# Kernel tuning notes

Hardware: AMD Instinct MI355X
Metric: run time of the kernel (lower is better)

The kernel has to match this reference:

```python
import jax, jax.numpy as jnp
import numpy as np

BATCH, IN, HID, OUT = 8192, 1024, 2048, 1024


def setup_inputs() -> dict:
    key = jax.random.key(0)
    ks = jax.random.split(key, 13)
    s = 0.02
    return {
        "x": jax.random.normal(ks[0], (BATCH, IN), jnp.float32),
        "hidden": jax.random.normal(ks[1], (BATCH, HID), jnp.float32),
        # torch nn.Linear stores weight as (out_features, in_features)
        "Wxr_w": jax.random.normal(ks[2], (HID, IN), jnp.float32) * s,
        "Wxr_b": jax.random.normal(ks[3], (HID,), jnp.float32) * s,
        "Whr_w": jax.random.normal(ks[4], (HID, HID), jnp.float32) * s,
        "Wxz_w": jax.random.normal(ks[5], (HID, IN), jnp.float32) * s,
        "Wxz_b": jax.random.normal(ks[6], (HID,), jnp.float32) * s,
        "Whz_w": jax.random.normal(ks[7], (HID, HID), jnp.float32) * s,
        "Wxh_w": jax.random.normal(ks[8], (HID, IN), jnp.float32) * s,
        "Wxh_b": jax.random.normal(ks[9], (HID,), jnp.float32) * s,
        "Whh_w": jax.random.normal(ks[10], (HID, HID), jnp.float32) * s,
        "Who_w": jax.random.normal(ks[11], (OUT, HID), jnp.float32) * s,
        "Who_b": jax.random.normal(ks[12], (OUT,), jnp.float32) * s,
    }


def _lin(x, w, b=None):
    y = x @ w.T
    return y if b is None else y + b


def reference(x, hidden, Wxr_w, Wxr_b, Whr_w, Wxz_w, Wxz_b, Whz_w,
              Wxh_w, Wxh_b, Whh_w, Who_w, Who_b):
    # GRU cell, one timestep
    r = jax.nn.sigmoid(_lin(x, Wxr_w, Wxr_b) + _lin(hidden, Whr_w))      # reset gate (B,H)
    z = jax.nn.sigmoid(_lin(x, Wxz_w, Wxz_b) + _lin(hidden, Whz_w))      # update gate (B,H)
    h_cand = jnp.tanh(_lin(x, Wxh_w, Wxh_b) + _lin(r * hidden, Whh_w))    # candidate (B,H)
    new_hidden = z * hidden + (1.0 - z) * h_cand                          # blend (B,H)
    output = _lin(new_hidden, Who_w, Who_b)                               # (B,OUT)
    return (output, new_hidden)
```

## Files before the change

### kernel.cpp

```cpp
#include <hip/hip_runtime.h>
#include <hip/hip_bf16.h>
#include <stdint.h>

typedef __bf16 bf16_t;
typedef __bf16 bf16x8 __attribute__((ext_vector_type(8)));
typedef float f32x4 __attribute__((ext_vector_type(4)));

#define B_SZ   8192
#define D_IN   1024
#define D_HID  2048
#define D_OUT  1024

#define BM 128
#define BN 128
#define BK 64

struct CastJobs {
  const float* src[9];
  bf16_t* dst[9];
  int n8[9];
};

__global__ __launch_bounds__(256) void cast_kernel(CastJobs j) {
  const int which = blockIdx.y;
  const int t = blockIdx.x * 256 + threadIdx.x;
  if (t >= j.n8[which]) return;
  const float4* s = (const float4*)j.src[which];
  float4 a = s[2 * t], b = s[2 * t + 1];
  bf16x8 o;
  o[0] = (bf16_t)a.x; o[1] = (bf16_t)a.y; o[2] = (bf16_t)a.z; o[3] = (bf16_t)a.w;
  o[4] = (bf16_t)b.x; o[5] = (bf16_t)b.y; o[6] = (bf16_t)b.z; o[7] = (bf16_t)b.w;
  *(bf16x8*)(j.dst[which] + (size_t)t * 8) = o;
}

__device__ __forceinline__ void stage_tile(const bf16_t* __restrict__ src, int ld,
                                           int row_base, int col_base,
                                           char* tile, int wid, int lane) {
#pragma unroll
  for (int i = 0; i < 4; ++i) {
    int p = i * 4096 + wid * 1024 + lane * 16;
    int row = p >> 7;
    int chunk = ((p >> 4) & 7) ^ (row & 7);
    const bf16_t* g = src + (size_t)(row_base + row) * ld + col_base + chunk * 8;
    __builtin_amdgcn_global_load_lds(
        (const __attribute__((address_space(1))) void*)g,
        (__attribute__((address_space(3))) void*)(tile + i * 4096 + wid * 1024),
        16, 0, 0);
  }
}

__device__ __forceinline__ bf16x8 read_frag(const char* tile, int row, int k) {
  int slot = (k >> 3) ^ (row & 7);
  return *(const bf16x8*)(tile + row * 128 + slot * 16);
}

__device__ __forceinline__ float sigm(float x) { return 1.0f / (1.0f + __expf(-x)); }

template <int MODE>
__global__ __launch_bounds__(256, 2) void gru_gemm(
    const bf16_t* __restrict__ xb, const bf16_t* __restrict__ hb,
    const bf16_t* __restrict__ wxr, const bf16_t* __restrict__ whr,
    const bf16_t* __restrict__ wxz, const bf16_t* __restrict__ whz,
    const bf16_t* __restrict__ wxh, const bf16_t* __restrict__ whh,
    const bf16_t* __restrict__ who,
    const float* __restrict__ bxr, const float* __restrict__ bxz,
    const float* __restrict__ bxh, const float* __restrict__ bwo,
    const float* __restrict__ hidden_f32,
    bf16_t* __restrict__ rh, bf16_t* __restrict__ zb, bf16_t* __restrict__ hx,
    bf16_t* __restrict__ nhb, float* __restrict__ out_y, float* __restrict__ out_nh) {
  __shared__ char lds[32768];
  char* sA = lds;
  char* sB = lds + 16384;

  const int tid = threadIdx.x;
  const int wid = tid >> 6;
  const int lane = tid & 63;
  const int wr = wid >> 1, wc = wid & 1;
  const int l15 = lane & 15, lq = lane >> 4;

  const int bm = blockIdx.x * BM;
  int region = 0, bn;
  if (MODE == 0) { region = blockIdx.y >> 4; bn = (blockIdx.y & 15) * BN; }
  else bn = blockIdx.y * BN;

  int KT;
  const bf16_t *BX = nullptr, *BH = nullptr;
  if (MODE == 0) {
    if (region == 0)      { BX = wxr; BH = whr; KT = D_IN + D_HID; }
    else if (region == 1) { BX = wxz; BH = whz; KT = D_IN + D_HID; }
    else                  { BX = wxh;           KT = D_IN; }
  } else {
    KT = D_HID;
  }

  f32x4 acc[4][4];
#pragma unroll
  for (int i = 0; i < 4; ++i)
#pragma unroll
    for (int j = 0; j < 4; ++j) acc[i][j] = (f32x4){0.f, 0.f, 0.f, 0.f};

  for (int kt = 0; kt < KT; kt += BK) {
    const bf16_t *As, *Bs;
    int lda, ldb, ac, bc;
    if (MODE == 0) {
      if (kt < D_IN) { As = xb; lda = D_IN;  ac = kt;        Bs = BX; ldb = D_IN;  bc = kt; }
      else           { As = hb; lda = D_HID; ac = kt - D_IN; Bs = BH; ldb = D_HID; bc = kt - D_IN; }
    } else if (MODE == 1) { As = rh;  lda = D_HID; ac = kt; Bs = whh; ldb = D_HID; bc = kt; }
    else                  { As = nhb; lda = D_HID; ac = kt; Bs = who; ldb = D_HID; bc = kt; }

    stage_tile(As, lda, bm, ac, sA, wid, lane);
    stage_tile(Bs, ldb, bn, bc, sB, wid, lane);
    asm volatile("s_waitcnt vmcnt(0)" ::: "memory");
    __syncthreads();

#pragma unroll
    for (int kk = 0; kk < BK; kk += 32) {
      bf16x8 af[4], bfr[4];
      const int k = kk + lq * 8;
#pragma unroll
      for (int i = 0; i < 4; ++i) af[i]  = read_frag(sA, wr * 64 + i * 16 + l15, k);
#pragma unroll
      for (int i = 0; i < 4; ++i) bfr[i] = read_frag(sB, wc * 64 + i * 16 + l15, k);
#pragma unroll
      for (int mi = 0; mi < 4; ++mi)
#pragma unroll
        for (int ni = 0; ni < 4; ++ni)
          acc[mi][ni] = __builtin_amdgcn_mfma_f32_16x16x32_bf16(af[mi], bfr[ni], acc[mi][ni], 0, 0, 0);
    }
    __syncthreads();
  }

#pragma unroll
  for (int ni = 0; ni < 4; ++ni) {
    const int col = bn + wc * 64 + ni * 16 + l15;
#pragma unroll
    for (int mi = 0; mi < 4; ++mi) {
      const int row0 = bm + wr * 64 + mi * 16 + lq * 4;
#pragma unroll
      for (int j = 0; j < 4; ++j) {
        const int row = row0 + j;
        const float v = acc[mi][ni][j];
        if (MODE == 0) {
          const size_t off = (size_t)row * D_HID + col;
          if (region == 0) {
            float rr = sigm(v + bxr[col]);
            rh[off] = (bf16_t)(rr * hidden_f32[off]);
          } else if (region == 1) {
            zb[off] = (bf16_t)sigm(v + bxz[col]);
          } else {
            hx[off] = (bf16_t)(v + bxh[col]);
          }
        } else if (MODE == 1) {
          const size_t off = (size_t)row * D_HID + col;
          float hc = tanhf((float)hx[off] + v);
          float z = (float)zb[off];
          float h = hidden_f32[off];
          float nh = z * h + (1.0f - z) * hc;
          out_nh[off] = nh;
          nhb[off] = (bf16_t)nh;
        } else {
          out_y[(size_t)row * D_OUT + col] = v + bwo[col];
        }
      }
    }
  }
}

extern "C" void kernel_launch(void* const* d_in, const int* in_sizes, int n_in,
                              void* d_out, int out_size, void* d_ws, size_t ws_size,
                              hipStream_t stream) {
  const float* x   = (const float*)d_in[0];
  const float* hid = (const float*)d_in[1];
  const float* Wxr = (const float*)d_in[2];
  const float* bxr = (const float*)d_in[3];
  const float* Whr = (const float*)d_in[4];
  const float* Wxz = (const float*)d_in[5];
  const float* bxz = (const float*)d_in[6];
  const float* Whz = (const float*)d_in[7];
  const float* Wxh = (const float*)d_in[8];
  const float* bxh = (const float*)d_in[9];
  const float* Whh = (const float*)d_in[10];
  const float* Who = (const float*)d_in[11];
  const float* bwo = (const float*)d_in[12];

  float* out_y  = (float*)d_out;
  float* out_nh = out_y + (size_t)B_SZ * D_OUT;

  char* w = (char*)d_ws;
  auto alloc = [&](size_t bytes) { char* p = w; w += (bytes + 255) & ~(size_t)255; return p; };

  bf16_t* xb  = (bf16_t*)alloc((size_t)B_SZ * D_IN * 2);
  bf16_t* hb  = (bf16_t*)alloc((size_t)B_SZ * D_HID * 2);
  bf16_t* wxr = (bf16_t*)alloc((size_t)D_HID * D_IN * 2);
  bf16_t* whr = (bf16_t*)alloc((size_t)D_HID * D_HID * 2);
  bf16_t* wxz = (bf16_t*)alloc((size_t)D_HID * D_IN * 2);
  bf16_t* whz = (bf16_t*)alloc((size_t)D_HID * D_HID * 2);
  bf16_t* wxh = (bf16_t*)alloc((size_t)D_HID * D_IN * 2);
  bf16_t* whh = (bf16_t*)alloc((size_t)D_HID * D_HID * 2);
  bf16_t* who = (bf16_t*)alloc((size_t)D_OUT * D_HID * 2);
  bf16_t* rh  = (bf16_t*)alloc((size_t)B_SZ * D_HID * 2);
  bf16_t* zb  = (bf16_t*)alloc((size_t)B_SZ * D_HID * 2);
  bf16_t* hx  = (bf16_t*)alloc((size_t)B_SZ * D_HID * 2);
  bf16_t* nhb = (bf16_t*)alloc((size_t)B_SZ * D_HID * 2);

  CastJobs cj;
  const float* srcs[9] = {x, hid, Wxr, Whr, Wxz, Whz, Wxh, Whh, Who};
  bf16_t* dsts[9]      = {xb, hb, wxr, whr, wxz, whz, wxh, whh, who};
  const int ns[9] = {B_SZ * D_IN, B_SZ * D_HID,
                     D_HID * D_IN, D_HID * D_HID,
                     D_HID * D_IN, D_HID * D_HID,
                     D_HID * D_IN, D_HID * D_HID,
                     D_OUT * D_HID};
  for (int i = 0; i < 9; ++i) { cj.src[i] = srcs[i]; cj.dst[i] = dsts[i]; cj.n8[i] = ns[i] / 8; }

  cast_kernel<<<dim3(8192, 9), dim3(256), 0, stream>>>(cj);

  dim3 blk(256);
  gru_gemm<0><<<dim3(64, 48), blk, 0, stream>>>(xb, hb, wxr, whr, wxz, whz, wxh, whh, who,
                                                bxr, bxz, bxh, bwo, hid,
                                                rh, zb, hx, nhb, out_y, out_nh);
  gru_gemm<1><<<dim3(64, 16), blk, 0, stream>>>(xb, hb, wxr, whr, wxz, whz, wxh, whh, who,
                                                bxr, bxz, bxh, bwo, hid,
                                                rh, zb, hx, nhb, out_y, out_nh);
  gru_gemm<2><<<dim3(64, 8), blk, 0, stream>>>(xb, hb, wxr, whr, wxz, whz, wxh, whh, who,
                                               bxr, bxz, bxh, bwo, hid,
                                               rh, zb, hx, nhb, out_y, out_nh);
}
```

Baseline: 758.2 us.

## Use 256x256 eight-wave GEMM with double-buffered LDS pipeline for gate GEMMs

Replaces the 128x128 single-buffered GEMM for the gate and candidate stages with a 512-thread, 256x256 tile kernel. It double-buffers LDS (128KB), interleaves async global-to-LDS staging of the next K tiles with MFMA phases on quarter sub-tiles, and raises wave priority around the MFMA blocks. It also remaps workgroup IDs so consecutive blocks spread across XCDs. The aim is to hide global load latency and increase data reuse per loaded byte. The cost is heavy LDS use, which limits occupancy, and fewer blocks for the tail-heavy region-2 work. The output projection keeps the old simple kernel.

New measurement: 956.7 us. 26.2% more time.

```diff
diff --git a/kernel.cpp b/kernel.cpp
--- a/kernel.cpp
+++ b/kernel.cpp
@@ -11,9 +11,7 @@
 #define D_HID  2048
 #define D_OUT  1024
 
-#define BM 128
-#define BN 128
-#define BK 64
+__device__ __forceinline__ float sigm(float x) { return 1.0f / (1.0f + __expf(-x)); }
 
 struct CastJobs {
   const float* src[9];
@@ -33,41 +31,177 @@
   *(bf16x8*)(j.dst[which] + (size_t)t * 8) = o;
 }
 
-__device__ __forceinline__ void stage_tile(const bf16_t* __restrict__ src, int ld,
-                                           int row_base, int col_base,
-                                           char* tile, int wid, int lane) {
-#pragma unroll
-  for (int i = 0; i < 4; ++i) {
-    int p = i * 4096 + wid * 1024 + lane * 16;
-    int row = p >> 7;
-    int chunk = ((p >> 4) & 7) ^ (row & 7);
-    const bf16_t* g = src + (size_t)(row_base + row) * ld + col_base + chunk * 8;
-    __builtin_amdgcn_global_load_lds(
-        (const __attribute__((address_space(1))) void*)g,
-        (__attribute__((address_space(3))) void*)(tile + i * 4096 + wid * 1024),
-        16, 0, 0);
-  }
-}
-
-__device__ __forceinline__ bf16x8 read_frag(const char* tile, int row, int k) {
-  int slot = (k >> 3) ^ (row & 7);
-  return *(const bf16x8*)(tile + row * 128 + slot * 16);
-}
-
-__device__ __forceinline__ float sigm(float x) { return 1.0f / (1.0f + __expf(-x)); }
-
 template <int MODE>
-__global__ __launch_bounds__(256, 2) void gru_gemm(
+__global__ __launch_bounds__(512, 2) void gru_gemm8(
     const bf16_t* __restrict__ xb, const bf16_t* __restrict__ hb,
     const bf16_t* __restrict__ wxr, const bf16_t* __restrict__ whr,
     const bf16_t* __restrict__ wxz, const bf16_t* __restrict__ whz,
     const bf16_t* __restrict__ wxh, const bf16_t* __restrict__ whh,
-    const bf16_t* __restrict__ who,
     const float* __restrict__ bxr, const float* __restrict__ bxz,
-    const float* __restrict__ bxh, const float* __restrict__ bwo,
+    const float* __restrict__ bxh,
     const float* __restrict__ hidden_f32,
     bf16_t* __restrict__ rh, bf16_t* __restrict__ zb, bf16_t* __restrict__ hx,
-    bf16_t* __restrict__ nhb, float* __restrict__ out_y, float* __restrict__ out_nh) {
+    bf16_t* __restrict__ nhb, float* __restrict__ out_nh) {
+  __shared__ char lds[131072];
+
+  const int tid = threadIdx.x;
+  const int wid = tid >> 6, lane = tid & 63;
+  const int wr = wid >> 2, wc = wid & 3;
+  const int l15 = lane & 15, lq = lane >> 4;
+
+  const int nbx = 32;
+  const int nby = (MODE == 0) ? 24 : 8;
+  const int nwg = nbx * nby;
+  int flat = blockIdx.y * nbx + blockIdx.x;
+  flat = (flat & 7) * (nwg >> 3) + (flat >> 3);
+  const int bx = flat & 31, by = flat >> 5;
+  const int bm = bx * 256;
+  int region = 0, bn;
+  if (MODE == 0) { region = by >> 3; bn = (by & 7) * 256; }
+  else bn = by * 256;
+
+  const int NT = (MODE == 0) ? (region == 2 ? 16 : 48) : 32;
+
+  auto srcA = [&](int t, const bf16_t*& p, int& ld, int& col) {
+    int kt = t * 64;
+    if (MODE == 0) {
+      if (kt < D_IN) { p = xb; ld = D_IN; col = kt; }
+      else { p = hb; ld = D_HID; col = kt - D_IN; }
+    } else { p = rh; ld = D_HID; col = kt; }
+  };
+  auto srcB = [&](int t, const bf16_t*& p, int& ld, int& col) {
+    int kt = t * 64;
+    if (MODE == 0) {
+      const bf16_t* BX = (region == 0) ? wxr : (region == 1) ? wxz : wxh;
+      if (region == 2 || kt < D_IN) { p = BX; ld = D_IN; col = kt; }
+      else { p = (region == 0) ? whr : whz; ld = D_HID; col = kt - D_IN; }
+    } else { p = whh; ld = D_HID; col = kt; }
+  };
+
+  auto stage = [&](const bf16_t* p, int ld, int rowbase, int col, char* ldsbase) {
+#pragma unroll
+    for (int i = 0; i < 2; ++i) {
+      int pp = i * 8192 + wid * 1024 + lane * 16;
+      int row = pp >> 7;
+      int chunk = ((pp >> 4) & 7) ^ (row & 7);
+      const bf16_t* g = p + (size_t)(rowbase + row) * ld + col + chunk * 8;
+      __builtin_amdgcn_global_load_lds(
+          (const __attribute__((address_space(1))) void*)g,
+          (__attribute__((address_space(3))) void*)(ldsbase + i * 8192 + wid * 1024),
+          16, 0, 0);
+    }
+  };
+  auto stageA = [&](int t, int half) {
+    const bf16_t* p; int ld, col; srcA(t, p, ld, col);
+    stage(p, ld, bm + half * 128, col, lds + (t & 1) * 32768 + half * 16384);
+  };
+  auto stageB = [&](int t, int half) {
+    const bf16_t* p; int ld, col; srcB(t, p, ld, col);
+    stage(p, ld, bn + half * 128, col, lds + 65536 + (t & 1) * 32768 + half * 16384);
+  };
+
+  auto readA = [&](int cur, int mh, int mi, int ks) {
+    int row = wr * 64 + mi * 16 + l15;
+    int chunk = (ks * 4 + lq) ^ (l15 & 7);
+    return *(const bf16x8*)(lds + cur * 32768 + mh * 16384 + row * 128 + chunk * 16);
+  };
+  auto readB = [&](int cur, int nh, int ni, int ks) {
+    int row = wc * 32 + ni * 16 + l15;
+    int chunk = (ks * 4 + lq) ^ (l15 & 7);
+    return *(const bf16x8*)(lds + 65536 + cur * 32768 + nh * 16384 + row * 128 + chunk * 16);
+  };
+
+  f32x4 acc[4][4][2];
+#pragma unroll
+  for (int j = 0; j < 4; ++j)
+#pragma unroll
+    for (int mi = 0; mi < 4; ++mi)
+#pragma unroll
+      for (int ni = 0; ni < 2; ++ni) acc[j][mi][ni] = (f32x4){0.f, 0.f, 0.f, 0.f};
+
+  bf16x8 af[4][2], bfr[2][2];
+
+  stageA(0, 0); stageB(0, 0); stageA(0, 1); stageB(0, 1);
+  if (NT > 1) { stageA(1, 0); stageB(1, 1); }
+  asm volatile("s_waitcnt vmcnt(4)" ::: "memory");
+  __builtin_amdgcn_s_barrier();
+
+  for (int t = 0; t < NT; ++t) {
+    const int cur = t & 1;
+#define GRU_PHASE(J, MH, NH, LA, LB, STG)                                   \
+    {                                                                        \
+      if (LA) {                                                              \
+        _Pragma("unroll") for (int mi = 0; mi < 4; ++mi)                     \
+        _Pragma("unroll") for (int ks = 0; ks < 2; ++ks)                     \
+          af[mi][ks] = readA(cur, MH, mi, ks);                               \
+      }                                                                      \
+      if (LB) {                                                              \
+        _Pragma("unroll") for (int ni = 0; ni < 2; ++ni)                     \
+        _Pragma("unroll") for (int ks = 0; ks < 2; ++ks)                     \
+          bfr[ni][ks] = readB(cur, NH, ni, ks);                              \
+      }                                                                      \
+      STG;                                                                   \
+      __builtin_amdgcn_s_barrier();                                          \
+      asm volatile("s_waitcnt lgkmcnt(0)" ::: "memory");                     \
+      __builtin_amdgcn_s_setprio(1);                                         \
+      _Pragma("unroll") for (int mi = 0; mi < 4; ++mi)                       \
+      _Pragma("unroll") for (int ni = 0; ni < 2; ++ni)                       \
+      _Pragma("unroll") for (int ks = 0; ks < 2; ++ks)                       \
+        acc[J][mi][ni] = __builtin_amdgcn_mfma_f32_16x16x32_bf16(            \
+            af[mi][ks], bfr[ni][ks], acc[J][mi][ni], 0, 0, 0);               \
+      __builtin_amdgcn_s_setprio(0);                                         \
+      if (J == 3) { asm volatile("s_waitcnt vmcnt(4)" ::: "memory"); }       \
+      __builtin_amdgcn_s_barrier();                                          \
+    }
+
+    GRU_PHASE(0, 0, 0, true,  true,  { if (t + 1 < NT) stageB(t + 1, 0); })
+    GRU_PHASE(1, 0, 1, false, true,  { if (t + 1 < NT) stageA(t + 1, 1); })
+    GRU_PHASE(2, 1, 1, true,  false, { if (t + 2 < NT) stageA(t + 2, 0); })
+    GRU_PHASE(3, 1, 0, false, true,  { if (t + 2 < NT) stageB(t + 2, 1); })
+#undef GRU_PHASE
+  }
+
+#pragma unroll
+  for (int j = 0; j < 4; ++j) {
+    const int mh = (j >= 2) ? 1 : 0;
+    const int nh = (j == 1 || j == 2) ? 1 : 0;
+#pragma unroll
+    for (int ni = 0; ni < 2; ++ni) {
+      const int col = bn + nh * 128 + wc * 32 + ni * 16 + l15;
+#pragma unroll
+      for (int mi = 0; mi < 4; ++mi) {
+        const int row0 = bm + mh * 128 + wr * 64 + mi * 16 + lq * 4;
+#pragma unroll
+        for (int r = 0; r < 4; ++r) {
+          const int row = row0 + r;
+          const float v = acc[j][mi][ni][r];
+          const size_t off = (size_t)row * D_HID + col;
+          if (MODE == 0) {
+            if (region == 0) {
+              float rr = sigm(v + bxr[col]);
+              rh[off] = (bf16_t)(rr * hidden_f32[off]);
+            } else if (region == 1) {
+              zb[off] = (bf16_t)sigm(v + bxz[col]);
+            } else {
+              hx[off] = (bf16_t)(v + bxh[col]);
+            }
+          } else {
+            float hc = tanhf((float)hx[off] + v);
+            float z = (float)zb[off];
+            float h = hidden_f32[off];
+            float nh2 = z * h + (1.0f - z) * hc;
+            out_nh[off] = nh2;
+            nhb[off] = (bf16_t)nh2;
+          }
+        }
+      }
+    }
+  }
+}
+
+__global__ __launch_bounds__(256, 2) void gru_gemm_out(
+    const bf16_t* __restrict__ nhb, const bf16_t* __restrict__ who,
+    const float* __restrict__ bwo, float* __restrict__ out_y) {
   __shared__ char lds[32768];
   char* sA = lds;
   char* sB = lds + 16384;
@@ -78,20 +212,8 @@
   const int wr = wid >> 1, wc = wid & 1;
   const int l15 = lane & 15, lq = lane >> 4;
 
-  const int bm = blockIdx.x * BM;
-  int region = 0, bn;
-  if (MODE == 0) { region = blockIdx.y >> 4; bn = (blockIdx.y & 15) * BN; }
-  else bn = blockIdx.y * BN;
-
-  int KT;
-  const bf16_t *BX = nullptr, *BH = nullptr;
-  if (MODE == 0) {
-    if (region == 0)      { BX = wxr; BH = whr; KT = D_IN + D_HID; }
-    else if (region == 1) { BX = wxz; BH = whz; KT = D_IN + D_HID; }
-    else                  { BX = wxh;           KT = D_IN; }
-  } else {
-    KT = D_HID;
-  }
+  const int bm = blockIdx.x * 128;
+  const int bn = blockIdx.y * 128;
 
   f32x4 acc[4][4];
 #pragma unroll
@@ -99,33 +221,43 @@
 #pragma unroll
     for (int j = 0; j < 4; ++j) acc[i][j] = (f32x4){0.f, 0.f, 0.f, 0.f};
 
-  for (int kt = 0; kt < KT; kt += BK) {
-    const bf16_t *As, *Bs;
-    int lda, ldb, ac, bc;
-    if (MODE == 0) {
-      if (kt < D_IN) { As = xb; lda = D_IN;  ac = kt;        Bs = BX; ldb = D_IN;  bc = kt; }
-      else           { As = hb; lda = D_HID; ac = kt - D_IN; Bs = BH; ldb = D_HID; bc = kt - D_IN; }
-    } else if (MODE == 1) { As = rh;  lda = D_HID; ac = kt; Bs = whh; ldb = D_HID; bc = kt; }
-    else                  { As = nhb; lda = D_HID; ac = kt; Bs = who; ldb = D_HID; bc = kt; }
-
-    stage_tile(As, lda, bm, ac, sA, wid, lane);
-    stage_tile(Bs, ldb, bn, bc, sB, wid, lane);
+  auto stage_tile = [&](const bf16_t* src, int ld, int row_base, int col_base, char* tile) {
+#pragma unroll
+    for (int i = 0; i < 4; ++i) {
+      int p = i * 4096 + wid * 1024 + lane * 16;
+      int row = p >> 7;
+      int chunk = ((p >> 4) & 7) ^ (row & 7);
+      const bf16_t* g = src + (size_t)(row_base + row) * ld + col_base + chunk * 8;
+      __builtin_amdgcn_global_load_lds(
+          (const __attribute__((address_space(1))) void*)g,
+          (__attribute__((address_space(3))) void*)(tile + i * 4096 + wid * 1024),
+          16, 0, 0);
+    }
+  };
+  auto read_frag = [&](const char* tile, int row, int k) {
+    int slot = (k >> 3) ^ (row & 7);
+    return *(const bf16x8*)(tile + row * 128 + slot * 16);
+  };
+
+  for (int kt = 0; kt < D_HID; kt += 64) {
+    stage_tile(nhb, D_HID, bm, kt, sA);
+    stage_tile(who, D_HID, bn, kt, sB);
     asm volatile("s_waitcnt vmcnt(0)" ::: "memory");
     __syncthreads();
 
 #pragma unroll
-    for (int kk = 0; kk < BK; kk += 32) {
-      bf16x8 af[4], bfr[4];
+    for (int kk = 0; kk < 64; kk += 32) {
+      bf16x8 af[4], bfv[4];
       const int k = kk + lq * 8;
 #pragma unroll
       for (int i = 0; i < 4; ++i) af[i]  = read_frag(sA, wr * 64 + i * 16 + l15, k);
 #pragma unroll
-      for (int i = 0; i < 4; ++i) bfr[i] = read_frag(sB, wc * 64 + i * 16 + l15, k);
+      for (int i = 0; i < 4; ++i) bfv[i] = read_frag(sB, wc * 64 + i * 16 + l15, k);
 #pragma unroll
       for (int mi = 0; mi < 4; ++mi)
 #pragma unroll
         for (int ni = 0; ni < 4; ++ni)
-          acc[mi][ni] = __builtin_amdgcn_mfma_f32_16x16x32_bf16(af[mi], bfr[ni], acc[mi][ni], 0, 0, 0);
+          acc[mi][ni] = __builtin_amdgcn_mfma_f32_16x16x32_bf16(af[mi], bfv[ni], acc[mi][ni], 0, 0, 0);
     }
     __syncthreads();
   }
@@ -137,31 +269,8 @@
     for (int mi = 0; mi < 4; ++mi) {
       const int row0 = bm + wr * 64 + mi * 16 + lq * 4;
 #pragma unroll
-      for (int j = 0; j < 4; ++j) {
-        const int row = row0 + j;
-        const float v = acc[mi][ni][j];
-        if (MODE == 0) {
-          const size_t off = (size_t)row * D_HID + col;
-          if (region == 0) {
-            float rr = sigm(v + bxr[col]);
-            rh[off] = (bf16_t)(rr * hidden_f32[off]);
-          } else if (region == 1) {
-            zb[off] = (bf16_t)sigm(v + bxz[col]);
-          } else {
-            hx[off] = (bf16_t)(v + bxh[col]);
-          }
-        } else if (MODE == 1) {
-          const size_t off = (size_t)row * D_HID + col;
-          float hc = tanhf((float)hx[off] + v);
-          float z = (float)zb[off];
-          float h = hidden_f32[off];
-          float nh = z * h + (1.0f - z) * hc;
-          out_nh[off] = nh;
-          nhb[off] = (bf16_t)nh;
-        } else {
-          out_y[(size_t)row * D_OUT + col] = v + bwo[col];
-        }
-      }
+      for (int j = 0; j < 4; ++j)
+        out_y[(size_t)(row0 + j) * D_OUT + col] = acc[mi][ni][j] + bwo[col];
     }
   }
 }
@@ -215,14 +324,11 @@
 
   cast_kernel<<<dim3(8192, 9), dim3(256), 0, stream>>>(cj);
 
-  dim3 blk(256);
-  gru_gemm<0><<<dim3(64, 48), blk, 0, stream>>>(xb, hb, wxr, whr, wxz, whz, wxh, whh, who,
-                                                bxr, bxz, bxh, bwo, hid,
-                                                rh, zb, hx, nhb, out_y, out_nh);
-  gru_gemm<1><<<dim3(64, 16), blk, 0, stream>>>(xb, hb, wxr, whr, wxz, whz, wxh, whh, who,
-                                                bxr, bxz, bxh, bwo, hid,
-                                                rh, zb, hx, nhb, out_y, out_nh);
-  gru_gemm<2><<<dim3(64, 8), blk, 0, stream>>>(xb, hb, wxr, whr, wxz, whz, wxh, whh, who,
-                                               bxr, bxz, bxh, bwo, hid,
-                                               rh, zb, hx, nhb, out_y, out_nh);
+  gru_gemm8<0><<<dim3(32, 24), dim3(512), 0, stream>>>(
+      xb, hb, wxr, whr, wxz, whz, wxh, whh,
+      bxr, bxz, bxh, hid, rh, zb, hx, nhb, out_nh);
+  gru_gemm8<1><<<dim3(32, 8), dim3(512), 0, stream>>>(
+      xb, hb, wxr, whr, wxz, whz, wxh, whh,
+      bxr, bxz, bxh, hid, rh, zb, hx, nhb, out_nh);
+  gru_gemm_out<<<dim3(64, 8), dim3(256), 0, stream>>>(nhb, who, bwo, out_y);
 }
```
